# Kernel optimization log

Hardware: AMD Instinct MI355X
Metric: run time of the kernel (lower is better)

The kernel has to match this reference:

```python
import jax, jax.numpy as jnp
import numpy as np

HEADS, K = 8, 32
EPS = 1e-5


def bn(x, gamma, beta):
    # batch-stat BN over all axes except the last (channel) axis
    axes = tuple(range(x.ndim - 1))
    m = jnp.mean(x, axes, keepdims=True)
    v = jnp.var(x, axes, keepdims=True)
    return (x - m) / jnp.sqrt(v + EPS) * gamma + beta


def leaky(z):
    return jax.nn.leaky_relu(z, 0.2)


def conv1(t, W, g, b):  # 1x1 Conv1d + BN + LeakyReLU, channels-last
    return leaky(bn(jnp.einsum('bnc,dc->bnd', t, W), g, b))


def conv2(t, W, g, b):  # 1x1 Conv2d + BN + LeakyReLU on (B,N,k,C)
    return leaky(bn(jnp.einsum('bnkc,dc->bnkd', t, W), g, b))


def _forward(x, pos, Wq, gq, bq, Wk, gk, bk, Wv, gv, bv,
             Wpb, gpb, bpb, We1, ge1, be1, We2, ge2, be2,
             Wm1, gm1, bm1, Wm2, gm2, bm2):
    B, N, C = x.shape
    cph = C // HEADS
    q = conv1(x, Wq, gq, bq)
    key = conv1(x, Wk, gk, bk)
    val = conv1(x, Wv, gv, bv)
    # kNN in key-feature space (DGCNN-style get_graph_feature, edge_function='global')
    sq = jnp.sum(key * key, -1)                          # (B,N)
    dist = sq[:, :, None] + sq[:, None, :] - 2.0 * jnp.einsum('bnc,bmc->bnm', key, key)
    _, idx = jax.lax.top_k(-dist, K)                     # (B,N,K)
    bidx = jnp.arange(B)[:, None, None]
    key_nb = key[bidx, idx]                              # (B,N,K,C)
    val_nb = val[bidx, idx]
    pos_nb = pos[bidx, idx]
    mask = jnp.sign(idx + 1).astype(x.dtype)             # (B,N,K), all ones for valid knn
    masked_pos = (pos_nb - pos[:, :, None, :]) * mask[..., None]
    posb = conv2(masked_pos, Wpb, gpb, bpb)              # (B,N,K,C)
    vector = key_nb - q[:, :, None, :] + posb            # vector attention logits input
    value = val_nb + posb
    vector = conv2(conv2(vector, We1, ge1, be1), We2, ge2, be2)  # (B,N,K,cph)
    vector = jax.nn.softmax(vector, axis=2) * mask[..., None]    # softmax over k neighbors
    value = value.reshape(B, N, K, cph, HEADS)
    attn = jnp.einsum('bnkgh,bnkg->bngh', value, vector).reshape(B, N, C)
    x = x + attn
    h = jax.nn.silu(bn(jnp.einsum('bnc,dc->bnd', x, Wm1), gm1, bm1))
    m = jax.nn.silu(bn(jnp.einsum('bnc,dc->bnd', h, Wm2), gm2, bm2))
    return x + m


def setup_inputs():
    key = jax.random.key(0)
    ks = jax.random.split(key, 16)
    B, N, C, H = 2, 2048, 256, 512
    cph = C // HEADS
    s = 0.02
    inp = {
        'x': jax.random.normal(ks[0], (B, N, C), jnp.float32),
        'pos': jax.random.normal(ks[1], (B, N, C), jnp.float32),
        'Wq': jax.random.normal(ks[2], (C, C), jnp.float32) * s,
        'gq': jnp.ones((C,), jnp.float32), 'bq': jnp.zeros((C,), jnp.float32),
        'Wk': jax.random.normal(ks[3], (C, C), jnp.float32) * s,
        'gk': jnp.ones((C,), jnp.float32), 'bk': jnp.zeros((C,), jnp.float32),
        'Wv': jax.random.normal(ks[4], (C, C), jnp.float32) * s,
        'gv': jnp.ones((C,), jnp.float32), 'bv': jnp.zeros((C,), jnp.float32),
        'Wpb': jax.random.normal(ks[5], (C, C), jnp.float32) * s,
        'gpb': jnp.ones((C,), jnp.float32), 'bpb': jnp.zeros((C,), jnp.float32),
        'We1': jax.random.normal(ks[6], (cph, C), jnp.float32) * s,
        'ge1': jnp.ones((cph,), jnp.float32), 'be1': jnp.zeros((cph,), jnp.float32),
        'We2': jax.random.normal(ks[7], (cph, cph), jnp.float32) * s,
        'ge2': jnp.ones((cph,), jnp.float32), 'be2': jnp.zeros((cph,), jnp.float32),
        'Wm1': jax.random.normal(ks[8], (H, C), jnp.float32) * s,
        'gm1': jnp.ones((H,), jnp.float32), 'bm1': jnp.zeros((H,), jnp.float32),
        'Wm2': jax.random.normal(ks[9], (C, H), jnp.float32) * s,
        'gm2': jnp.ones((C,), jnp.float32), 'bm2': jnp.zeros((C,), jnp.float32),
    }
    return inp


def reference(x, pos, Wq, gq, bq, Wk, gk, bk, Wv, gv, bv,
              Wpb, gpb, bpb, We1, ge1, be1, We2, ge2, be2,
              Wm1, gm1, bm1, Wm2, gm2, bm2):
    return _forward(x, pos, Wq, gq, bq, Wk, gk, bk, Wv, gv, bv,
                    Wpb, gpb, bpb, We1, ge1, be1, We2, ge2, be2,
                    Wm1, gm1, bm1, Wm2, gm2, bm2)
```

## Files before the change

### kernel.cpp

```cpp
#include <hip/hip_runtime.h>

#define EPS 1e-5f

typedef __attribute__((ext_vector_type(8))) short s8v;
typedef __attribute__((ext_vector_type(4))) float f4v;

__device__ __forceinline__ float leakyf(float z){ return z >= 0.f ? z : 0.2f*z; }
__device__ __forceinline__ float siluf(float y){ return y / (1.f + __expf(-y)); }
__device__ __forceinline__ unsigned f2bfu(float f){
  unsigned u = __float_as_uint(f);
  return (u + 0x7FFFu + ((u>>16)&1u)) >> 16;
}
__device__ __forceinline__ unsigned short bfr(float f){ return (unsigned short)f2bfu(f); }
__device__ __forceinline__ float bf2f16(unsigned short s){ return __uint_as_float(((unsigned)s)<<16); }

__global__ __launch_bounds__(256) void k_zero(float* __restrict__ p, int n){
  int i = blockIdx.x*256 + threadIdx.x;
  if (i < n) p[i] = 0.f;
}

template<bool TRANSA, bool STATS>
__global__ __launch_bounds__(256) void k_gemm(
    const float* __restrict__ A, int lda,
    const float* __restrict__ A3, int lda3,
    const float* __restrict__ fAbuck, float invnA, int CA,
    const float* __restrict__ gA, const float* __restrict__ bA,
    const float* __restrict__ B0, const float* __restrict__ B1,
    const float* __restrict__ B2, const float* __restrict__ B3, int ldb,
    float* __restrict__ C, int ldc, long cStr,
    float* __restrict__ C3, int ldc3,
    int K, float* __restrict__ buck, int statC, int statChanStr)
{
  __shared__ unsigned short Ah[2048], Al[2048], Bh[2048], Bl[2048];
  __shared__ float Ssum[64], Ssq[64];
  __shared__ float mrA[1024];
  const int z = blockIdx.z;
  const bool zAlt = (A3 != nullptr) && (z == 3);
  const float* Az = zAlt ? A3 : A;
  const int ldaz = zAlt ? lda3 : lda;
  const float* Bb = (z==0?B0 : z==1?B1 : (z==2?B2:B3));
  float* Cb = zAlt ? C3 : (C + (long)z*cStr);
  const int ldcz = zAlt ? ldc3 : ldc;
  const bool doStats = STATS && !zAlt;
  const int tid = threadIdx.x;
  const int bm = blockIdx.x*64, bn = blockIdx.y*64;
  const int wv = tid>>6, lane = tid&63;
  const int lm = lane&15, quad = lane>>4;
  if (doStats && tid<64){ Ssum[tid]=0.f; Ssq[tid]=0.f; }
  if (TRANSA){
    for (int c = tid; c < CA; c += 256){
      float s=0.f, q=0.f;
      for (int b=0;b<64;b++){ s += fAbuck[(long)b*2*CA + c]; q += fAbuck[(long)b*2*CA + CA + c]; }
      float m = s*invnA;
      float v = fmaxf(q*invnA - m*m, 0.f);
      mrA[c] = m; mrA[CA + c] = rsqrtf(v + EPS);
    }
    __syncthreads();
  }

  const int r0 = tid>>3, kg = tid&7;
  const int qk = kg>>1, j0 = (kg&1)*4;
  const int s0 = ((((r0>>4)  )*4 + qk)*16 + ((r0&15)^qk))*8 + j0;
  const int s1 = ((((r0>>4)+2)*4 + qk)*16 + ((r0&15)^qk))*8 + j0;
  const float* aP0 = Az + (long)(bm+r0)*ldaz + kg*4;
  const float* aP1 = aP0 + (long)32*ldaz;
  const float* bP0 = Bb + (long)(bn+r0)*ldb + kg*4;
  const float* bP1 = bP0 + (long)32*ldb;

  f4v acc[4];
  #pragma unroll
  for (int j=0;j<4;j++) acc[j] = (f4v){0.f,0.f,0.f,0.f};

  float4 a0 = *(const float4*)(aP0);
  float4 a1 = *(const float4*)(aP1);
  float4 b0 = *(const float4*)(bP0);
  float4 b1 = *(const float4*)(bP1);

  for (int k0=0; k0<K; k0+=32){
    float4 av0 = a0, av1 = a1;
    if (TRANSA){
      float4 m4 = *(const float4*)&mrA[k0 + kg*4];
      float4 r4 = *(const float4*)&mrA[CA + k0 + kg*4];
      float4 g4 = *(const float4*)(gA + k0 + kg*4);
      float4 b4 = *(const float4*)(bA + k0 + kg*4);
      av0.x = siluf((av0.x - m4.x)*r4.x*g4.x + b4.x);
      av0.y = siluf((av0.y - m4.y)*r4.y*g4.y + b4.y);
      av0.z = siluf((av0.z - m4.z)*r4.z*g4.z + b4.z);
      av0.w = siluf((av0.w - m4.w)*r4.w*g4.w + b4.w);
      av1.x = siluf((av1.x - m4.x)*r4.x*g4.x + b4.x);
      av1.y = siluf((av1.y - m4.y)*r4.y*g4.y + b4.y);
      av1.z = siluf((av1.z - m4.z)*r4.z*g4.z + b4.z);
      av1.w = siluf((av1.w - m4.w)*r4.w*g4.w + b4.w);
    }
    ushort4 h4, l4;
    h4.x=bfr(av0.x); l4.x=bfr(av0.x-bf2f16(h4.x));
    h4.y=bfr(av0.y); l4.y=bfr(av0.y-bf2f16(h4.y));
    h4.z=bfr(av0.z); l4.z=bfr(av0.z-bf2f16(h4.z));
    h4.w=bfr(av0.w); l4.w=bfr(av0.w-bf2f16(h4.w));
    *(ushort4*)&Ah[s0]=h4; *(ushort4*)&Al[s0]=l4;
    h4.x=bfr(av1.x); l4.x=bfr(av1.x-bf2f16(h4.x));
    h4.y=bfr(av1.y); l4.y=bfr(av1.y-bf2f16(h4.y));
    h4.z=bfr(av1.z); l4.z=bfr(av1.z-bf2f16(h4.z));
    h4.w=bfr(av1.w); l4.w=bfr(av1.w-bf2f16(h4.w));
    *(ushort4*)&Ah[s1]=h4; *(ushort4*)&Al[s1]=l4;
    h4.x=bfr(b0.x); l4.x=bfr(b0.x-bf2f16(h4.x));
    h4.y=bfr(b0.y); l4.y=bfr(b0.y-bf2f16(h4.y));
    h4.z=bfr(b0.z); l4.z=bfr(b0.z-bf2f16(h4.z));
    h4.w=bfr(b0.w); l4.w=bfr(b0.w-bf2f16(h4.w));
    *(ushort4*)&Bh[s0]=h4; *(ushort4*)&Bl[s0]=l4;
    h4.x=bfr(b1.x); l4.x=bfr(b1.x-bf2f16(h4.x));
    h4.y=bfr(b1.y); l4.y=bfr(b1.y-bf2f16(h4.y));
    h4.z=bfr(b1.z); l4.z=bfr(b1.z-bf2f16(h4.z));
    h4.w=bfr(b1.w); l4.w=bfr(b1.w-bf2f16(h4.w));
    *(ushort4*)&Bh[s1]=h4; *(ushort4*)&Bl[s1]=l4;
    __syncthreads();
    if (k0+32 < K){
      a0 = *(const float4*)(aP0 + k0+32);
      a1 = *(const float4*)(aP1 + k0+32);
      b0 = *(const float4*)(bP0 + k0+32);
      b1 = *(const float4*)(bP1 + k0+32);
    }
    const int soA = ((wv*4 + quad)*16 + (lm^quad))*8;
    s8v ah = *(const s8v*)&Ah[soA];
    s8v al = *(const s8v*)&Al[soA];
    #pragma unroll
    for (int j=0;j<4;j++){
      const int soB = ((j*4 + quad)*16 + (lm^quad))*8;
      s8v bh = *(const s8v*)&Bh[soB];
      s8v bl = *(const s8v*)&Bl[soB];
      acc[j] = __builtin_amdgcn_mfma_f32_16x16x32_bf16(ah, bh, acc[j], 0,0,0);
      acc[j] = __builtin_amdgcn_mfma_f32_16x16x32_bf16(ah, bl, acc[j], 0,0,0);
      acc[j] = __builtin_amdgcn_mfma_f32_16x16x32_bf16(al, bh, acc[j], 0,0,0);
      acc[j] = __builtin_amdgcn_mfma_f32_16x16x32_bf16(al, bl, acc[j], 0,0,0);
    }
    __syncthreads();
  }
  #pragma unroll
  for (int rr=0;rr<4;rr++){
    float* cr = Cb + (long)(bm + wv*16 + quad*4 + rr)*ldcz + bn + lm;
    #pragma unroll
    for (int j=0;j<4;j++) cr[j*16] = acc[j][rr];
  }
  if (doStats){
    #pragma unroll
    for (int j=0;j<4;j++){
      float s=0.f, q=0.f;
      #pragma unroll
      for (int rr=0;rr<4;rr++){ float v = acc[j][rr]; s += v; q += v*v; }
      s += __shfl_xor(s,16,64); s += __shfl_xor(s,32,64);
      q += __shfl_xor(q,16,64); q += __shfl_xor(q,32,64);
      if (quad==0){ atomicAdd(&Ssum[j*16+lm], s); atomicAdd(&Ssq[j*16+lm], q); }
    }
    __syncthreads();
    if (tid < 64){
      int chan = statChanStr*z + bn + tid;
      float* bb = buck + (long)(blockIdx.x & 63)*2*statC;
      atomicAdd(&bb[chan], Ssum[tid]);
      atomicAdd(&bb[statC + chan], Ssq[tid]);
    }
  }
}

__global__ void k_finalize(const float* __restrict__ buck, int C, float invn, float* __restrict__ mr){
  int c = blockIdx.x*256 + threadIdx.x;
  if (c < C){
    float s=0,q=0;
    for (int b=0;b<64;b++){ s += buck[(long)b*2*C + c]; q += buck[(long)b*2*C + C + c]; }
    float m = s*invn;
    float v = fmaxf(q*invn - m*m, 0.f);
    mr[c] = m; mr[C+c] = rsqrtf(v + EPS);
  }
}

__global__ __launch_bounds__(256) void k_apply_qkv(const float* __restrict__ raw, const float* __restrict__ mr,
    const float* __restrict__ gq, const float* __restrict__ bq,
    const float* __restrict__ gk, const float* __restrict__ bk,
    const float* __restrict__ gv, const float* __restrict__ bv,
    float* __restrict__ key, float* __restrict__ qv, float* __restrict__ sq){
  const int r = blockIdx.x, tid = threadIdx.x;
  __shared__ float red[256];
  const float* row = raw + (long)r*768;
  float zq = row[tid], zk = row[256+tid], zv = row[512+tid];
  float yq = leakyf((zq - mr[tid])*mr[768+tid]*gq[tid] + bq[tid]);
  float yk = leakyf((zk - mr[256+tid])*mr[1024+tid]*gk[tid] + bk[tid]);
  float yv = leakyf((zv - mr[512+tid])*mr[1280+tid]*gv[tid] + bv[tid]);
  qv[(long)r*512 + tid] = yq;
  key[(long)r*256 + tid] = yk;
  qv[(long)r*512 + 256 + tid] = yv;
  red[tid] = yk*yk; __syncthreads();
  for (int off=128; off; off>>=1){ if (tid<off) red[tid] += red[tid+off]; __syncthreads(); }
  if (tid==0) sq[r] = red[0];
}

__global__ __launch_bounds__(256) void k_topk(const float* __restrict__ G, const float* __restrict__ sqb,
    int* __restrict__ idxb){
  __shared__ float dist[4][2048];
  const int wv = threadIdx.x >> 6, lane = threadIdx.x & 63;
  const int n = blockIdx.x*4 + wv;
  const float* Grow = G + (long)n*2048;
  const float sqn = sqb[n];
  float lmin = 3.4e38f; int lidx = 0;
  for (int j=0;j<32;j++){
    int m = lane + j*64;
    float d = sqn + sqb[m] - 2.f*Grow[m];
    dist[wv][m] = d;
    if (d < lmin){ lmin = d; lidx = m; }
  }
  int* orow = idxb + n*32;
  for (int t=0;t<32;t++){
    float v = lmin; int i = lidx;
    for (int off=32; off; off>>=1){
      float v2 = __shfl_xor(v, off, 64);
      int i2 = __shfl_xor(i, off, 64);
      if (v2 < v || (v2 == v && i2 < i)){ v = v2; i = i2; }
    }
    if (lane == 0) orow[t] = i;
    if ((i & 63) == lane){
      dist[wv][i] = 3.4e38f;
      lmin = 3.4e38f; lidx = 0;
      for (int j=0;j<32;j++){
        int m = lane + j*64;
        float d = dist[wv][m];
        if (d < lmin){ lmin = d; lidx = m; }
      }
    }
  }
}

__global__ __launch_bounds__(256) void k_stats_pb(const float* __restrict__ P, const int* __restrict__ idx,
    float* __restrict__ buck){
  const int c = threadIdx.x;
  float s=0,q=0;
  for (int r = blockIdx.x; r < 4096; r += gridDim.x){
    const long base = (long)(r >> 11) << 11;
    const float pn = P[(long)r*256 + c];
    const int* ir = idx + r*32;
    for (int k=0;k<32;k++){
      int g = ir[k];
      float z = P[(base + g)*256 + c] - pn;
      s += z; q += z*z;
    }
  }
  float* bb = buck + (long)(blockIdx.x & 63)*512;
  atomicAdd(&bb[c], s); atomicAdd(&bb[256+c], q);
}

__global__ __launch_bounds__(256) void k_e1m(
    const float* __restrict__ key, const float* __restrict__ qv, const float* __restrict__ P,
    const int* __restrict__ idx, const float* __restrict__ mrPB,
    const float* __restrict__ gpb, const float* __restrict__ bpb,
    const float* __restrict__ We1, float* __restrict__ E1, float* __restrict__ buckE1)
{
  __shared__ unsigned short Ab[16384];
  __shared__ unsigned short Wb[8192];
  __shared__ float Ssum[32], Ssq[32];
  const int tid = threadIdx.x;
  const int wv = tid>>6, lane = tid&63;
  const int quad = lane>>4, lm = lane&15;
  const int bn0 = blockIdx.x*2;
  if (tid < 32){ Ssum[tid]=0.f; Ssq[tid]=0.f; }
  for (int e = tid; e < 8192; e += 256){
    int d = e >> 8, c = e & 255;
    int off = (((d>>4)*8 + (c>>5))*4 + ((c>>3)&3))*128 + (d&15)*8 + (c&7);
    Wb[off] = bfr(We1[e]);
  }
  {
    const int bn = bn0 + (wv>>1);
    const long base = (long)(bn >> 11) << 11;
    const int c4 = lane*4;
    float4 q4  = *(const float4*)(qv + (long)bn*512 + c4);
    float4 pn4 = *(const float4*)(P + (long)bn*256 + c4);
    float4 mp4 = *(const float4*)(mrPB + c4);
    float4 rp4 = *(const float4*)(mrPB + 256 + c4);
    float4 g4  = *(const float4*)(gpb + c4);
    float4 b4  = *(const float4*)(bpb + c4);
    const int ksc = c4>>5, quadc = (c4>>3)&3, jc = c4&7;
    for (int j = 0; j < 16; ++j){
      const int rloc = wv*16 + j;
      const int kk = rloc & 31;
      const int g = idx[bn*32 + kk];
      float4 kb = *(const float4*)(key + (base+g)*256 + c4);
      float4 pb = *(const float4*)(P + (base+g)*256 + c4);
      float o0 = kb.x - q4.x + leakyf((pb.x - pn4.x - mp4.x)*rp4.x*g4.x + b4.x);
      float o1 = kb.y - q4.y + leakyf((pb.y - pn4.y - mp4.y)*rp4.y*g4.y + b4.y);
      float o2 = kb.z - q4.z + leakyf((pb.z - pn4.z - mp4.z)*rp4.z*g4.z + b4.z);
      float o3 = kb.w - q4.w + leakyf((pb.w - pn4.w - mp4.w)*rp4.w*g4.w + b4.w);
      const int atile = rloc >> 4;
      const int slot = ((rloc & 15) ^ (ksc<<1) ^ quadc) & 15;
      const int off = ((atile*8 + ksc)*4 + quadc)*128 + slot*8 + jc;
      ushort4 u; u.x = bfr(o0); u.y = bfr(o1); u.z = bfr(o2); u.w = bfr(o3);
      *(ushort4*)&Ab[off] = u;
    }
  }
  __syncthreads();
  f4v acc0 = (f4v){0,0,0,0}, acc1 = (f4v){0,0,0,0};
  #pragma unroll
  for (int ks=0; ks<8; ks++){
    const int aslot = (lm ^ (ks<<1) ^ quad) & 15;
    s8v a  = *(const s8v*)&Ab[((wv*8 + ks)*4 + quad)*128 + aslot*8];
    s8v b0 = *(const s8v*)&Wb[((ks)*4 + quad)*128 + lm*8];
    s8v b1 = *(const s8v*)&Wb[((8 + ks)*4 + quad)*128 + lm*8];
    acc0 = __builtin_amdgcn_mfma_f32_16x16x32_bf16(a, b0, acc0, 0,0,0);
    acc1 = __builtin_amdgcn_mfma_f32_16x16x32_bf16(a, b1, acc1, 0,0,0);
  }
  {
    const int bn = bn0 + (wv>>1);
    const int mt = wv & 1;
    #pragma unroll
    for (int rr=0; rr<4; rr++){
      int krow = mt*16 + quad*4 + rr;
      float* o = E1 + ((long)bn*32 + krow)*32;
      o[lm]      = acc0[rr];
      o[16 + lm] = acc1[rr];
    }
  }
  float s0=0,q0=0,s1=0,q1=0;
  #pragma unroll
  for (int rr=0; rr<4; rr++){
    s0 += acc0[rr]; q0 += acc0[rr]*acc0[rr];
    s1 += acc1[rr]; q1 += acc1[rr]*acc1[rr];
  }
  s0 += __shfl_xor(s0,16,64); s0 += __shfl_xor(s0,32,64);
  q0 += __shfl_xor(q0,16,64); q0 += __shfl_xor(q0,32,64);
  s1 += __shfl_xor(s1,16,64); s1 += __shfl_xor(s1,32,64);
  q1 += __shfl_xor(q1,16,64); q1 += __shfl_xor(q1,32,64);
  if (quad == 0){
    atomicAdd(&Ssum[lm], s0);      atomicAdd(&Ssq[lm], q0);
    atomicAdd(&Ssum[16+lm], s1);   atomicAdd(&Ssq[16+lm], q1);
  }
  __syncthreads();
  if (tid < 32){
    float* bb = buckE1 + (long)(blockIdx.x & 63)*64;
    atomicAdd(&bb[tid], Ssum[tid]); atomicAdd(&bb[32+tid], Ssq[tid]);
  }
}

__global__ __launch_bounds__(256) void k_e2m(
    float* __restrict__ E, const float* __restrict__ bE1buck,
    const float* __restrict__ ge1, const float* __restrict__ be1,
    const float* __restrict__ We2, float* __restrict__ buckE2)
{
  __shared__ unsigned short Ab[8192];
  __shared__ unsigned short Wb[1024];
  __shared__ float Ssum[32], Ssq[32];
  __shared__ float mrE1s[64];
  const int tid = threadIdx.x;
  const int wv = tid>>6, lane = tid&63;
  const int quad = lane>>4, lm = lane&15;
  const long r0 = (long)blockIdx.x*256;
  if (tid < 32){
    Ssum[tid]=0.f; Ssq[tid]=0.f;
    float s=0.f, q=0.f;
    for (int b=0;b<64;b++){ s += bE1buck[b*64+tid]; q += bE1buck[b*64+32+tid]; }
    float m = s*(1.f/131072.f);
    float v = fmaxf(q*(1.f/131072.f) - m*m, 0.f);
    mrE1s[tid] = m; mrE1s[32+tid] = rsqrtf(v + EPS);
  }
  for (int e = tid; e < 1024; e += 256){
    int d = e>>5, c = e&31;
    int off = ((d>>4)*4 + ((c>>3)&3))*128 + (d&15)*8 + (c&7);
    Wb[off] = bfr(We2[e]);
  }
  __syncthreads();
  #pragma unroll
  for (int it=0; it<8; it++){
    int e = (tid + it*256)*4;
    int row = e>>5, c = e&31;
    float4 v = *(const float4*)(E + (r0 + row)*32 + c);
    float4 m4 = *(const float4*)&mrE1s[c];
    float4 r4 = *(const float4*)&mrE1s[32+c];
    float4 g4 = *(const float4*)(ge1 + c);
    float4 b4 = *(const float4*)(be1 + c);
    float o0 = leakyf((v.x - m4.x)*r4.x*g4.x + b4.x);
    float o1 = leakyf((v.y - m4.y)*r4.y*g4.y + b4.y);
    float o2 = leakyf((v.z - m4.z)*r4.z*g4.z + b4.z);
    float o3 = leakyf((v.w - m4.w)*r4.w*g4.w + b4.w);
    int quadc = (c>>3)&3, jc = c&7;
    int slot = ((row&15) ^ quadc) & 15;
    int off = ((row>>4)*4 + quadc)*128 + slot*8 + jc;
    ushort4 u; u.x=bfr(o0); u.y=bfr(o1); u.z=bfr(o2); u.w=bfr(o3);
    *(ushort4*)&Ab[off] = u;
  }
  __syncthreads();
  f4v acc0[4], acc1[4];
  #pragma unroll
  for (int i=0;i<4;i++){ acc0[i]=(f4v){0,0,0,0}; acc1[i]=(f4v){0,0,0,0}; }
  const int aslot = (lm ^ quad) & 15;
  s8v b0 = *(const s8v*)&Wb[(quad)*128 + lm*8];
  s8v b1 = *(const s8v*)&Wb[(4 + quad)*128 + lm*8];
  #pragma unroll
  for (int i=0;i<4;i++){
    const int atile = wv*4 + i;
    s8v a = *(const s8v*)&Ab[(atile*4 + quad)*128 + aslot*8];
    acc0[i] = __builtin_amdgcn_mfma_f32_16x16x32_bf16(a, b0, acc0[i], 0,0,0);
    acc1[i] = __builtin_amdgcn_mfma_f32_16x16x32_bf16(a, b1, acc1[i], 0,0,0);
  }
  __syncthreads();
  float s0=0,q0=0,s1=0,q1=0;
  #pragma unroll
  for (int i=0;i<4;i++){
    const int atile = wv*4 + i;
    #pragma unroll
    for (int rr=0; rr<4; rr++){
      long row = r0 + atile*16 + quad*4 + rr;
      float* o = E + row*32;
      o[lm]      = acc0[i][rr];
      o[16 + lm] = acc1[i][rr];
      s0 += acc0[i][rr]; q0 += acc0[i][rr]*acc0[i][rr];
      s1 += acc1[i][rr]; q1 += acc1[i][rr]*acc1[i][rr];
    }
  }
  s0 += __shfl_xor(s0,16,64); s0 += __shfl_xor(s0,32,64);
  q0 += __shfl_xor(q0,16,64); q0 += __shfl_xor(q0,32,64);
  s1 += __shfl_xor(s1,16,64); s1 += __shfl_xor(s1,32,64);
  q1 += __shfl_xor(q1,16,64); q1 += __shfl_xor(q1,32,64);
  if (quad == 0){
    atomicAdd(&Ssum[lm], s0);    atomicAdd(&Ssq[lm], q0);
    atomicAdd(&Ssum[16+lm], s1); atomicAdd(&Ssq[16+lm], q1);
  }
  __syncthreads();
  if (tid < 32){
    float* bb = buckE2 + (long)(blockIdx.x & 63)*64;
    atomicAdd(&bb[tid], Ssum[tid]); atomicAdd(&bb[32+tid], Ssq[tid]);
  }
}

__global__ __launch_bounds__(256) void k_attn(
    const float* __restrict__ E2, const float* __restrict__ bE2buck,
    const float* __restrict__ ge2, const float* __restrict__ be2,
    const float* __restrict__ qv, const float* __restrict__ P, const int* __restrict__ idx,
    const float* __restrict__ mrPB, const float* __restrict__ gpb, const float* __restrict__ bpb,
    const float* __restrict__ xin, float* __restrict__ x2)
{
  __shared__ float L[4][32][33];
  __shared__ float mrE2s[64];
  const int tid = threadIdx.x;
  const int wv = tid>>6, lane = tid&63;
  if (tid < 32){
    float s=0.f, q=0.f;
    for (int b=0;b<64;b++){ s += bE2buck[b*64+tid]; q += bE2buck[b*64+32+tid]; }
    float m = s*(1.f/131072.f);
    float v = fmaxf(q*(1.f/131072.f) - m*m, 0.f);
    mrE2s[tid] = m; mrE2s[32+tid] = rsqrtf(v + EPS);
  }
  __syncthreads();
  const int bn = blockIdx.x*4 + wv;
  const long base = (long)(bn >> 11) << 11;
  for (int qq=0; qq<4; qq++){
    int e = lane*16 + qq*4;
    int k = e >> 5, g0 = e & 31;
    float4 v  = *(const float4*)(E2 + (long)bn*1024 + e);
    float4 m4 = *(const float4*)&mrE2s[g0];
    float4 r4 = *(const float4*)&mrE2s[32+g0];
    float4 g4 = *(const float4*)(ge2 + g0);
    float4 b4 = *(const float4*)(be2 + g0);
    L[wv][k][g0+0] = leakyf((v.x - m4.x)*r4.x*g4.x + b4.x);
    L[wv][k][g0+1] = leakyf((v.y - m4.y)*r4.y*g4.y + b4.y);
    L[wv][k][g0+2] = leakyf((v.z - m4.z)*r4.z*g4.z + b4.z);
    L[wv][k][g0+3] = leakyf((v.w - m4.w)*r4.w*g4.w + b4.w);
  }
  __syncthreads();
  {
    const int g = lane & 31, h = lane >> 5;
    float mx = -3.4e38f;
    for (int j=0;j<16;j++) mx = fmaxf(mx, L[wv][h*16+j][g]);
    mx = fmaxf(mx, __shfl_xor(mx, 32, 64));
    float sm = 0.f, ev[16];
    for (int j=0;j<16;j++){ float e_ = __expf(L[wv][h*16+j][g] - mx); ev[j] = e_; sm += e_; }
    sm += __shfl_xor(sm, 32, 64);
    float inv = 1.f/sm;
    for (int j=0;j<16;j++) L[wv][h*16+j][g] = ev[j]*inv;
  }
  __syncthreads();
  const int c4 = lane*4, gg = lane >> 1;
  float4 pn4 = *(const float4*)(P + (long)bn*256 + c4);
  float4 mp4 = *(const float4*)(mrPB + c4);
  float4 rp4 = *(const float4*)(mrPB + 256 + c4);
  float4 g4 = *(const float4*)(gpb + c4);
  float4 b4 = *(const float4*)(bpb + c4);
  float accv[4] = {0,0,0,0};
  const int* ir = idx + bn*32;
  for (int k=0;k<32;k++){
    int gi = ir[k];
    float4 vv = *(const float4*)(qv + (long)(base+gi)*512 + 256 + c4);
    float4 pp = *(const float4*)(P + (base+gi)*256 + c4);
    float w = L[wv][k][gg];
    float zh0 = (pp.x - pn4.x - mp4.x)*rp4.x*g4.x + b4.x;
    float zh1 = (pp.y - pn4.y - mp4.y)*rp4.y*g4.y + b4.y;
    float zh2 = (pp.z - pn4.z - mp4.z)*rp4.z*g4.z + b4.z;
    float zh3 = (pp.w - pn4.w - mp4.w)*rp4.w*g4.w + b4.w;
    accv[0] = fmaf(vv.x + leakyf(zh0), w, accv[0]);
    accv[1] = fmaf(vv.y + leakyf(zh1), w, accv[1]);
    accv[2] = fmaf(vv.z + leakyf(zh2), w, accv[2]);
    accv[3] = fmaf(vv.w + leakyf(zh3), w, accv[3]);
  }
  float4 x4 = *(const float4*)(xin + (long)bn*256 + c4);
  float4 o;
  o.x = x4.x + accv[0]; o.y = x4.y + accv[1];
  o.z = x4.z + accv[2]; o.w = x4.w + accv[3];
  *(float4*)(x2 + (long)bn*256 + c4) = o;
}

__global__ __launch_bounds__(256) void k_final(const float* __restrict__ x2, const float* __restrict__ Zm2,
    const float* __restrict__ bM2buck, const float* __restrict__ gm, const float* __restrict__ bm,
    float* __restrict__ out){
  __shared__ float mrs[512];
  const int tid = threadIdx.x;
  {
    float s=0.f, q=0.f;
    for (int b=0;b<64;b++){ s += bM2buck[(long)b*512 + tid]; q += bM2buck[(long)b*512 + 256 + tid]; }
    float m = s*(1.f/4096.f);
    float v = fmaxf(q*(1.f/4096.f) - m*m, 0.f);
    mrs[tid] = m; mrs[256+tid] = rsqrtf(v + EPS);
  }
  __syncthreads();
  #pragma unroll
  for (int rr=0; rr<4; rr++){
    long r = (long)blockIdx.x*4 + rr;
    float z = Zm2[r*256 + tid];
    float y = (z - mrs[tid])*mrs[256+tid]*gm[tid] + bm[tid];
    out[r*256 + tid] = x2[r*256 + tid] + siluf(y);
  }
}

extern "C" void kernel_launch(void* const* d_in, const int* in_sizes, int n_in,
                              void* d_out, int out_size, void* d_ws, size_t ws_size,
                              hipStream_t stream){
  (void)in_sizes; (void)n_in; (void)out_size; (void)ws_size;
  const float* x   = (const float*)d_in[0];
  const float* pos = (const float*)d_in[1];
  const float* Wq  = (const float*)d_in[2];
  const float* gq  = (const float*)d_in[3];
  const float* bq  = (const float*)d_in[4];
  const float* Wk  = (const float*)d_in[5];
  const float* gk  = (const float*)d_in[6];
  const float* bk  = (const float*)d_in[7];
  const float* Wv  = (const float*)d_in[8];
  const float* gv  = (const float*)d_in[9];
  const float* bv  = (const float*)d_in[10];
  const float* Wpb = (const float*)d_in[11];
  const float* gpb = (const float*)d_in[12];
  const float* bpb = (const float*)d_in[13];
  const float* We1 = (const float*)d_in[14];
  const float* ge1 = (const float*)d_in[15];
  const float* be1 = (const float*)d_in[16];
  const float* We2 = (const float*)d_in[17];
  const float* ge2 = (const float*)d_in[18];
  const float* be2 = (const float*)d_in[19];
  const float* Wm1 = (const float*)d_in[20];
  const float* gm1 = (const float*)d_in[21];
  const float* bm1 = (const float*)d_in[22];
  const float* Wm2 = (const float*)d_in[23];
  const float* gm2 = (const float*)d_in[24];
  const float* bm2 = (const float*)d_in[25];

  float* w     = (float*)d_ws;
  float* arena = w;
  float* key   = w + 4194304;
  float* P     = w + 5242880;
  float* x2    = w + 6291456;
  float* qv    = w + 7340032;
  float* sq    = w + 9437184;
  int*   idx   = (int*)(w + 9441280);
  float* buck  = w + 9572352;
  float* mr    = w + 9809920;
  float* bQKV = buck;            float* bPB = buck + 98304;  float* bE1 = buck + 131072;
  float* bE2  = buck + 135168;   float* bM1 = buck + 139264; float* bM2 = buck + 204800;
  float* mrQKV = mr;        float* mrPB = mr + 1536;
  float* Zm1 = arena;
  float* Zm2 = arena + 2097152;

  k_zero<<<928,256,0,stream>>>(buck, 237568);
  k_gemm<false,true><<<dim3(64,4,4),256,0,stream>>>(
      x,256, pos,256, nullptr,0.f,0, nullptr,nullptr,
      Wq,Wk,Wv,Wpb,256, arena,768,256, P,256, 256, bQKV,768,256);
  k_finalize<<<3,256,0,stream>>>(bQKV, 768, 1.f/4096.f, mrQKV);
  k_apply_qkv<<<4096,256,0,stream>>>(arena, mrQKV, gq,bq,gk,bk,gv,bv, key, qv, sq);
  k_gemm<false,false><<<dim3(32,32,1),256,0,stream>>>(
      key,256, nullptr,0, nullptr,0.f,0, nullptr,nullptr,
      key,key,key,nullptr,256, arena,2048,0, nullptr,0, 256, nullptr,0,0);
  k_topk<<<512,256,0,stream>>>(arena, sq, idx);
  k_gemm<false,false><<<dim3(32,32,1),256,0,stream>>>(
      key+524288,256, nullptr,0, nullptr,0.f,0, nullptr,nullptr,
      key+524288,key+524288,key+524288,nullptr,256, arena,2048,0, nullptr,0, 256, nullptr,0,0);
  k_topk<<<512,256,0,stream>>>(arena, sq+2048, idx+65536);
  k_stats_pb<<<1024,256,0,stream>>>(P, idx, bPB);
  k_finalize<<<1,256,0,stream>>>(bPB, 256, 1.f/131072.f, mrPB);
  k_e1m<<<2048,256,0,stream>>>(key, qv, P, idx, mrPB, gpb, bpb, We1, arena, bE1);
  k_e2m<<<512,256,0,stream>>>(arena, bE1, ge1, be1, We2, bE2);
  k_attn<<<1024,256,0,stream>>>(arena, bE2, ge2, be2, qv, P, idx, mrPB, gpb, bpb, x, x2);
  k_gemm<false,true><<<dim3(64,8,1),256,0,stream>>>(
      x2,256, nullptr,0, nullptr,0.f,0, nullptr,nullptr,
      Wm1,Wm1,Wm1,nullptr,256, Zm1,512,0, nullptr,0, 256, bM1,512,0);
  k_gemm<true,true><<<dim3(64,4,1),256,0,stream>>>(
      Zm1,512, nullptr,0, bM1,1.f/4096.f,512, gm1,bm1,
      Wm2,Wm2,Wm2,nullptr,512, Zm2,256,0, nullptr,0, 512, bM2,256,0);
  k_final<<<1024,256,0,stream>>>(x2, Zm2, bM2, gm2, bm2, (float*)d_out);
}
```

Measured before the change: 372.6 us.

## Fuse launches: batch Gram GEMMs, fold stats into topk and finalize into apply

Both per-batch Gram GEMMs now run as one launch over grid z with strides into a separate buffer, so one topk launch covers both batches. The topk kernel also computes the position-bias BN statistics from its selected neighbours, which removes k_stats_pb. The QKV finalize is moved into k_apply_qkv, which now handles 8 rows per block with a shuffle reduction, and k_final handles 8 rows per block. The MLP GEMMs drop the low-by-low bf16 MFMA term, which lowers their precision in exchange for less matrix work.

```diff
diff --git a/kernel.cpp b/kernel.cpp
--- a/kernel.cpp
+++ b/kernel.cpp
@@ -19,26 +19,26 @@
   if (i < n) p[i] = 0.f;
 }
 
-template<bool TRANSA, bool STATS>
+template<bool TRANSA, bool STATS, bool FULL4>
 __global__ __launch_bounds__(256) void k_gemm(
-    const float* __restrict__ A, int lda,
+    const float* __restrict__ A, int lda, long aStr,
     const float* __restrict__ A3, int lda3,
     const float* __restrict__ fAbuck, float invnA, int CA,
     const float* __restrict__ gA, const float* __restrict__ bA,
     const float* __restrict__ B0, const float* __restrict__ B1,
-    const float* __restrict__ B2, const float* __restrict__ B3, int ldb,
+    const float* __restrict__ B2, const float* __restrict__ B3, int ldb, long bStr,
     float* __restrict__ C, int ldc, long cStr,
     float* __restrict__ C3, int ldc3,
     int K, float* __restrict__ buck, int statC, int statChanStr)
 {
   __shared__ unsigned short Ah[2048], Al[2048], Bh[2048], Bl[2048];
-  __shared__ float Ssum[64], Ssq[64];
-  __shared__ float mrA[1024];
+  __shared__ float Ssum[STATS?64:4], Ssq[STATS?64:4];
+  __shared__ float mrA[TRANSA?1024:4];
   const int z = blockIdx.z;
   const bool zAlt = (A3 != nullptr) && (z == 3);
-  const float* Az = zAlt ? A3 : A;
+  const float* Az = zAlt ? A3 : A + (long)z*aStr;
   const int ldaz = zAlt ? lda3 : lda;
-  const float* Bb = (z==0?B0 : z==1?B1 : (z==2?B2:B3));
+  const float* Bb = (z==0?B0 : z==1?B1 : (z==2?B2:B3)) + (long)z*bStr;
   float* Cb = zAlt ? C3 : (C + (long)z*cStr);
   const int ldcz = zAlt ? ldc3 : ldc;
   const bool doStats = STATS && !zAlt;
@@ -131,7 +131,8 @@
       acc[j] = __builtin_amdgcn_mfma_f32_16x16x32_bf16(ah, bh, acc[j], 0,0,0);
       acc[j] = __builtin_amdgcn_mfma_f32_16x16x32_bf16(ah, bl, acc[j], 0,0,0);
       acc[j] = __builtin_amdgcn_mfma_f32_16x16x32_bf16(al, bh, acc[j], 0,0,0);
-      acc[j] = __builtin_amdgcn_mfma_f32_16x16x32_bf16(al, bl, acc[j], 0,0,0);
+      if (FULL4)
+        acc[j] = __builtin_amdgcn_mfma_f32_16x16x32_bf16(al, bl, acc[j], 0,0,0);
     }
     __syncthreads();
   }
@@ -172,32 +173,53 @@
   }
 }
 
-__global__ __launch_bounds__(256) void k_apply_qkv(const float* __restrict__ raw, const float* __restrict__ mr,
+__global__ __launch_bounds__(256) void k_apply_qkv(const float* __restrict__ raw, const float* __restrict__ bQKV,
     const float* __restrict__ gq, const float* __restrict__ bq,
     const float* __restrict__ gk, const float* __restrict__ bk,
     const float* __restrict__ gv, const float* __restrict__ bv,
     float* __restrict__ key, float* __restrict__ qv, float* __restrict__ sq){
-  const int r = blockIdx.x, tid = threadIdx.x;
-  __shared__ float red[256];
-  const float* row = raw + (long)r*768;
-  float zq = row[tid], zk = row[256+tid], zv = row[512+tid];
-  float yq = leakyf((zq - mr[tid])*mr[768+tid]*gq[tid] + bq[tid]);
-  float yk = leakyf((zk - mr[256+tid])*mr[1024+tid]*gk[tid] + bk[tid]);
-  float yv = leakyf((zv - mr[512+tid])*mr[1280+tid]*gv[tid] + bv[tid]);
-  qv[(long)r*512 + tid] = yq;
-  key[(long)r*256 + tid] = yk;
-  qv[(long)r*512 + 256 + tid] = yv;
-  red[tid] = yk*yk; __syncthreads();
-  for (int off=128; off; off>>=1){ if (tid<off) red[tid] += red[tid+off]; __syncthreads(); }
-  if (tid==0) sq[r] = red[0];
-}
-
-__global__ __launch_bounds__(256) void k_topk(const float* __restrict__ G, const float* __restrict__ sqb,
-    int* __restrict__ idxb){
+  __shared__ float mrs[1536];
+  __shared__ float red[4];
+  const int tid = threadIdx.x;
+  const int wv = tid>>6, lane = tid&63;
+  for (int c = tid; c < 768; c += 256){
+    float s=0.f, q=0.f;
+    for (int b=0;b<64;b++){ s += bQKV[(long)b*1536 + c]; q += bQKV[(long)b*1536 + 768 + c]; }
+    float m = s*(1.f/4096.f);
+    float v = fmaxf(q*(1.f/4096.f) - m*m, 0.f);
+    mrs[c] = m; mrs[768+c] = rsqrtf(v + EPS);
+  }
+  __syncthreads();
+  const float gqv = gq[tid], bqv = bq[tid], gkv = gk[tid], bkv = bk[tid], gvv = gv[tid], bvv = bv[tid];
+  for (int rr=0; rr<8; rr++){
+    const long r = (long)blockIdx.x*8 + rr;
+    const float* row = raw + r*768;
+    float zq = row[tid], zk = row[256+tid], zv = row[512+tid];
+    float yq = leakyf((zq - mrs[tid])*mrs[768+tid]*gqv + bqv);
+    float yk = leakyf((zk - mrs[256+tid])*mrs[1024+tid]*gkv + bkv);
+    float yv = leakyf((zv - mrs[512+tid])*mrs[1280+tid]*gvv + bvv);
+    qv[r*512 + tid] = yq;
+    key[r*256 + tid] = yk;
+    qv[r*512 + 256 + tid] = yv;
+    float kq = yk*yk;
+    kq += __shfl_xor(kq,1,64); kq += __shfl_xor(kq,2,64);
+    kq += __shfl_xor(kq,4,64); kq += __shfl_xor(kq,8,64);
+    kq += __shfl_xor(kq,16,64); kq += __shfl_xor(kq,32,64);
+    if (lane==0) red[wv] = kq;
+    __syncthreads();
+    if (tid==0) sq[r] = red[0]+red[1]+red[2]+red[3];
+    __syncthreads();
+  }
+}
+
+__global__ __launch_bounds__(256) void k_topk(const float* __restrict__ G2, const float* __restrict__ sq,
+    int* __restrict__ idxb, const float* __restrict__ P, float* __restrict__ bPB){
   __shared__ float dist[4][2048];
   const int wv = threadIdx.x >> 6, lane = threadIdx.x & 63;
-  const int n = blockIdx.x*4 + wv;
-  const float* Grow = G + (long)n*2048;
+  const int row = blockIdx.x*4 + wv;
+  const int b = row >> 11, n = row & 2047;
+  const float* Grow = G2 + (long)b*4194304 + (long)n*2048;
+  const float* sqb = sq + b*2048;
   const float sqn = sqb[n];
   float lmin = 3.4e38f; int lidx = 0;
   for (int j=0;j<32;j++){
@@ -206,7 +228,8 @@
     dist[wv][m] = d;
     if (d < lmin){ lmin = d; lidx = m; }
   }
-  int* orow = idxb + n*32;
+  int* orow = idxb + row*32;
+  int myidx[32];
   for (int t=0;t<32;t++){
     float v = lmin; int i = lidx;
     for (int off=32; off; off>>=1){
@@ -214,6 +237,7 @@
       int i2 = __shfl_xor(i, off, 64);
       if (v2 < v || (v2 == v && i2 < i)){ v = v2; i = i2; }
     }
+    myidx[t] = i;
     if (lane == 0) orow[t] = i;
     if ((i & 63) == lane){
       dist[wv][i] = 3.4e38f;
@@ -225,24 +249,21 @@
       }
     }
   }
-}
-
-__global__ __launch_bounds__(256) void k_stats_pb(const float* __restrict__ P, const int* __restrict__ idx,
-    float* __restrict__ buck){
-  const int c = threadIdx.x;
-  float s=0,q=0;
-  for (int r = blockIdx.x; r < 4096; r += gridDim.x){
-    const long base = (long)(r >> 11) << 11;
-    const float pn = P[(long)r*256 + c];
-    const int* ir = idx + r*32;
-    for (int k=0;k<32;k++){
-      int g = ir[k];
-      float z = P[(base + g)*256 + c] - pn;
-      s += z; q += z*z;
-    }
-  }
-  float* bb = buck + (long)(blockIdx.x & 63)*512;
-  atomicAdd(&bb[c], s); atomicAdd(&bb[256+c], q);
+  const long base = (long)b << 11;
+  const int c4 = lane*4;
+  float4 pn = *(const float4*)(P + (long)row*256 + c4);
+  float s0=0,s1=0,s2=0,s3=0,q0=0,q1=0,q2=0,q3=0;
+  for (int t=0;t<32;t++){
+    float4 pg = *(const float4*)(P + (base + myidx[t])*256 + c4);
+    float z0 = pg.x - pn.x, z1 = pg.y - pn.y, z2 = pg.z - pn.z, z3 = pg.w - pn.w;
+    s0+=z0; q0+=z0*z0; s1+=z1; q1+=z1*z1;
+    s2+=z2; q2+=z2*z2; s3+=z3; q3+=z3*z3;
+  }
+  float* bb = bPB + (long)(blockIdx.x & 63)*512;
+  atomicAdd(&bb[c4+0], s0); atomicAdd(&bb[c4+1], s1);
+  atomicAdd(&bb[c4+2], s2); atomicAdd(&bb[c4+3], s3);
+  atomicAdd(&bb[256+c4+0], q0); atomicAdd(&bb[256+c4+1], q1);
+  atomicAdd(&bb[256+c4+2], q2); atomicAdd(&bb[256+c4+3], q3);
 }
 
 __global__ __launch_bounds__(256) void k_e1m(
@@ -514,11 +535,12 @@
     mrs[tid] = m; mrs[256+tid] = rsqrtf(v + EPS);
   }
   __syncthreads();
-  #pragma unroll
-  for (int rr=0; rr<4; rr++){
-    long r = (long)blockIdx.x*4 + rr;
+  const float gmv = gm[tid], bmv = bm[tid];
+  #pragma unroll
+  for (int rr=0; rr<8; rr++){
+    long r = (long)blockIdx.x*8 + rr;
     float z = Zm2[r*256 + tid];
-    float y = (z - mrs[tid])*mrs[256+tid]*gm[tid] + bm[tid];
+    float y = (z - mrs[tid])*mrs[256+tid]*gmv + bmv;
     out[r*256 + tid] = x2[r*256 + tid] + siluf(y);
   }
 }
@@ -564,36 +586,31 @@
   int*   idx   = (int*)(w + 9441280);
   float* buck  = w + 9572352;
   float* mr    = w + 9809920;
+  float* G2    = w + 9813632;
   float* bQKV = buck;            float* bPB = buck + 98304;  float* bE1 = buck + 131072;
   float* bE2  = buck + 135168;   float* bM1 = buck + 139264; float* bM2 = buck + 204800;
-  float* mrQKV = mr;        float* mrPB = mr + 1536;
+  float* mrPB = mr + 1536;
   float* Zm1 = arena;
   float* Zm2 = arena + 2097152;
 
   k_zero<<<928,256,0,stream>>>(buck, 237568);
-  k_gemm<false,true><<<dim3(64,4,4),256,0,stream>>>(
-      x,256, pos,256, nullptr,0.f,0, nullptr,nullptr,
-      Wq,Wk,Wv,Wpb,256, arena,768,256, P,256, 256, bQKV,768,256);
-  k_finalize<<<3,256,0,stream>>>(bQKV, 768, 1.f/4096.f, mrQKV);
-  k_apply_qkv<<<4096,256,0,stream>>>(arena, mrQKV, gq,bq,gk,bk,gv,bv, key, qv, sq);
-  k_gemm<false,false><<<dim3(32,32,1),256,0,stream>>>(
-      key,256, nullptr,0, nullptr,0.f,0, nullptr,nullptr,
-      key,key,key,nullptr,256, arena,2048,0, nullptr,0, 256, nullptr,0,0);
-  k_topk<<<512,256,0,stream>>>(arena, sq, idx);
-  k_gemm<false,false><<<dim3(32,32,1),256,0,stream>>>(
-      key+524288,256, nullptr,0, nullptr,0.f,0, nullptr,nullptr,
-      key+524288,key+524288,key+524288,nullptr,256, arena,2048,0, nullptr,0, 256, nullptr,0,0);
-  k_topk<<<512,256,0,stream>>>(arena, sq+2048, idx+65536);
-  k_stats_pb<<<1024,256,0,stream>>>(P, idx, bPB);
+  k_gemm<false,true,true><<<dim3(64,4,4),256,0,stream>>>(
+      x,256,0, pos,256, nullptr,0.f,0, nullptr,nullptr,
+      Wq,Wk,Wv,Wpb,256,0, arena,768,256, P,256, 256, bQKV,768,256);
+  k_apply_qkv<<<512,256,0,stream>>>(arena, bQKV, gq,bq,gk,bk,gv,bv, key, qv, sq);
+  k_gemm<false,false,true><<<dim3(32,32,2),256,0,stream>>>(
+      key,256,524288, nullptr,0, nullptr,0.f,0, nullptr,nullptr,
+      key,key,key,nullptr,256,524288, G2,2048,4194304, nullptr,0, 256, nullptr,0,0);
+  k_topk<<<1024,256,0,stream>>>(G2, sq, idx, P, bPB);
   k_finalize<<<1,256,0,stream>>>(bPB, 256, 1.f/131072.f, mrPB);
   k_e1m<<<2048,256,0,stream>>>(key, qv, P, idx, mrPB, gpb, bpb, We1, arena, bE1);
   k_e2m<<<512,256,0,stream>>>(arena, bE1, ge1, be1, We2, bE2);
   k_attn<<<1024,256,0,stream>>>(arena, bE2, ge2, be2, qv, P, idx, mrPB, gpb, bpb, x, x2);
-  k_gemm<false,true><<<dim3(64,8,1),256,0,stream>>>(
-      x2,256, nullptr,0, nullptr,0.f,0, nullptr,nullptr,
-      Wm1,Wm1,Wm1,nullptr,256, Zm1,512,0, nullptr,0, 256, bM1,512,0);
-  k_gemm<true,true><<<dim3(64,4,1),256,0,stream>>>(
-      Zm1,512, nullptr,0, bM1,1.f/4096.f,512, gm1,bm1,
-      Wm2,Wm2,Wm2,nullptr,512, Zm2,256,0, nullptr,0, 512, bM2,256,0);
-  k_final<<<1024,256,0,stream>>>(x2, Zm2, bM2, gm2, bm2, (float*)d_out);
-}
+  k_gemm<false,true,false><<<dim3(64,8,1),256,0,stream>>>(
+      x2,256,0, nullptr,0, nullptr,0.f,0, nullptr,nullptr,
+      Wm1,Wm1,Wm1,nullptr,256,0, Zm1,512,0, nullptr,0, 256, bM1,512,0);
+  k_gemm<true,true,false><<<dim3(64,4,1),256,0,stream>>>(
+      Zm1,512,0, nullptr,0, bM1,1.f/4096.f,512, gm1,bm1,
+      Wm2,Wm2,Wm2,nullptr,512,0, Zm2,256,0, nullptr,0, 512, bM2,256,0);
+  k_final<<<512,256,0,stream>>>(x2, Zm2, bM2, gm2, bm2, (float*)d_out);
+}
```

Result: faster. 358.1 us (-3.9%).
